# Optimization experiments

Measured on AMD Instinct MI355X. Metric: run time of the kernel, lower is better.

## Reference

```python
import jax, jax.numpy as jnp
import numpy as np

B, S, D, H = 4, 2048, 1024, 16
HD = D // H

def setup_inputs() -> dict:
    key = jax.random.key(0)
    ks = jax.random.split(key, 12)
    std = 1.0 / np.sqrt(D)
    inp = {
        'query': jax.random.normal(ks[0], (B, S, D), jnp.float32),
        'key':   jax.random.normal(ks[1], (B, S, D), jnp.float32),
        'value': jax.random.normal(ks[2], (B, S, D), jnp.float32),
        'mask':  jnp.tril(jnp.ones((S, S), jnp.int32))[None, None, :, :],  # [1,1,S,S] causal
        'Wq': jax.random.uniform(ks[3], (D, D), jnp.float32, -std, std),
        'bq': jax.random.uniform(ks[4], (D,), jnp.float32, -std, std),
        'Wk': jax.random.uniform(ks[5], (D, D), jnp.float32, -std, std),
        'bk': jax.random.uniform(ks[6], (D,), jnp.float32, -std, std),
        'Wv': jax.random.uniform(ks[7], (D, D), jnp.float32, -std, std),
        'bv': jax.random.uniform(ks[8], (D,), jnp.float32, -std, std),
        'Wo': jax.random.uniform(ks[9], (D, D), jnp.float32, -std, std),
        'bo': jax.random.uniform(ks[10], (D,), jnp.float32, -std, std),
    }
    return inp

def _split_heads(x, W, b):
    # torch Linear: x @ W.T + b ; then [B,S,H,HD] -> [B,H,S,HD]
    y = jnp.einsum('bsd,ed->bse', x, W) + b
    return y.reshape(x.shape[0], -1, H, HD).transpose(0, 2, 1, 3)

def reference(query, key, value, mask, Wq, bq, Wk, bk, Wv, bv, Wo, bo):
    q = _split_heads(query, Wq, bq)   # [B,H,S,HD]
    k = _split_heads(key,   Wk, bk)
    v = _split_heads(value, Wv, bv)
    logits = jnp.einsum('bhqd,bhkd->bhqk', q, k) / np.sqrt(HD)  # [B,H,S,S]
    logits = jnp.where(mask == 0, jnp.float32(-1e9), logits)
    attn = jax.nn.softmax(logits, axis=-1)
    out = jnp.einsum('bhqk,bhkd->bhqd', attn, v)               # [B,H,S,HD]
    out = out.transpose(0, 2, 1, 3).reshape(query.shape[0], -1, D)
    return jnp.einsum('bsd,ed->bse', out, Wo) + bo
```

## Files before the change

### kernel.cpp

```cpp
#include <hip/hip_runtime.h>
#include <hip/hip_bf16.h>


#define SLEN 2048
#define DMOD 1024

typedef __attribute__((ext_vector_type(8))) short s16x8;
typedef __attribute__((ext_vector_type(4))) float f32x4;

__device__ __forceinline__ unsigned short f2bf(float f) {
    union { __hip_bfloat16 h; unsigned short u; } cv;
    cv.h = __float2bfloat16(f);
    return cv.u;
}
__device__ __forceinline__ unsigned cvtpk(float a, float b) {
    unsigned r;
    asm("v_cvt_pk_bf16_f32 %0, %1, %2" : "=v"(r) : "v"(a), "v"(b));
    return r;
}

__device__ __forceinline__ void gload_lds16(const void* g, void* l) {
    __builtin_amdgcn_global_load_lds(
        (const __attribute__((address_space(1))) void*)g,
        (__attribute__((address_space(3))) void*)l, 16, 0, 0);
}

__global__ __launch_bounds__(256) void convert_w(
    const float* __restrict__ wq, const float* __restrict__ wk,
    const float* __restrict__ wv, const float* __restrict__ wo,
    unsigned short* __restrict__ dst)
{
    const int bid = blockIdx.x, tid = threadIdx.x;
    const int w = bid >> 7;
    const float* src = (w == 0) ? wq : (w == 1) ? wk : (w == 2) ? wv : wo;
    unsigned short* d = dst + (size_t)w * 1048576;
    const size_t off = (size_t)(bid & 127) * 8192;
#pragma unroll
    for (int i = 0; i < 8; ++i) {
        const size_t e = off + (size_t)(i * 256 + tid) * 4;
        float4 x = *reinterpret_cast<const float4*>(&src[e]);
        uint2 u;
        u.x = cvtpk(x.x, x.y);
        u.y = cvtpk(x.z, x.w);
        *reinterpret_cast<uint2*>(&d[e]) = u;
    }
}

template<int MODE>
__global__ __launch_bounds__(256) void gemm_qkv(
    const float* __restrict__ A, const unsigned short* __restrict__ W,
    const float* __restrict__ bias, unsigned short* __restrict__ outp,
    float oscale)
{
    __shared__ unsigned short Asm[2][8192];
    __shared__ unsigned short Bsm[2][8192];

    const int tid  = threadIdx.x;
    const int lane = tid & 63, wid = tid >> 6;
    const int l15 = lane & 15, lhi = lane >> 4;

    const int flat = blockIdx.x;
    const int logical = (flat & 7) * 64 + (flat >> 3);
    const int m0 = (logical >> 3) * 128, n0 = (logical & 7) * 128;
    const int wr = wid >> 1, wc = wid & 1;

    int soff[4];
    const float* aptc[4];
#pragma unroll
    for (int i = 0; i < 4; ++i) {
        const int f = i * 256 + tid;
        const int srow = f >> 3, sg = f & 7;
        soff[i] = srow * 128 + ((sg ^ (srow & 7)) * 16);
        aptc[i] = A + (size_t)(m0 + srow) * 1024 + sg * 8;
    }
    const int wsrow = lane >> 3;
    const int wsgr  = (lane & 7) ^ wsrow;
    const unsigned short* bpt = W + (size_t)(n0 + wid * 8 + wsrow) * 1024 + wsgr * 8;

    int aoff[2][4], boff[2][4];
#pragma unroll
    for (int kk = 0; kk < 2; ++kk)
#pragma unroll
        for (int i = 0; i < 4; ++i) {
            const int s = ((4 * kk + lhi) ^ (l15 & 7)) * 16;
            aoff[kk][i] = (wr * 64 + i * 16 + l15) * 128 + s;
            boff[kk][i] = (wc * 64 + i * 16 + l15) * 128 + s;
        }

    f32x4 acc[4][4];
#pragma unroll
    for (int i = 0; i < 4; ++i)
#pragma unroll
        for (int j = 0; j < 4; ++j) acc[i][j] = (f32x4)0.f;

    float4 aw[8];

    auto loadA = [&](int k0) {
#pragma unroll
        for (int i = 0; i < 4; ++i) {
            aw[2 * i]     = *reinterpret_cast<const float4*>(aptc[i] + k0);
            aw[2 * i + 1] = *reinterpret_cast<const float4*>(aptc[i] + k0 + 4);
        }
    };
    auto writeA = [&](int bsel) {
#pragma unroll
        for (int i = 0; i < 4; ++i) {
            uint4 u;
            u.x = cvtpk(aw[2 * i].x,     aw[2 * i].y);
            u.y = cvtpk(aw[2 * i].z,     aw[2 * i].w);
            u.z = cvtpk(aw[2 * i + 1].x, aw[2 * i + 1].y);
            u.w = cvtpk(aw[2 * i + 1].z, aw[2 * i + 1].w);
            *reinterpret_cast<uint4*>((char*)&Asm[bsel][0] + soff[i]) = u;
        }
    };
    auto stageW = [&](int bsel) {
        char* bd = (char*)Bsm + bsel * 16384 + wid * 1024;
#pragma unroll
        for (int i = 0; i < 4; ++i)
            gload_lds16(bpt + i * 32768, bd + i * 4096);
        bpt += 64;
    };

    loadA(0);
    stageW(0);
    writeA(0);
    __syncthreads();

#pragma unroll 1
    for (int kt = 0; kt < 16; ++kt) {
        if (kt < 15) {
            loadA((kt + 1) * 64);
            stageW((kt + 1) & 1);
        }
        const char* AB = (const char*)&Asm[kt & 1][0];
        const char* BB = (const char*)&Bsm[kt & 1][0];
#pragma unroll
        for (int kk = 0; kk < 2; ++kk) {
            s16x8 af[4], bfv[4];
#pragma unroll
            for (int i = 0; i < 4; ++i) af[i]  = *reinterpret_cast<const s16x8*>(AB + aoff[kk][i]);
#pragma unroll
            for (int j = 0; j < 4; ++j) bfv[j] = *reinterpret_cast<const s16x8*>(BB + boff[kk][j]);
#pragma unroll
            for (int i = 0; i < 4; ++i)
#pragma unroll
                for (int j = 0; j < 4; ++j)
                    acc[i][j] = __builtin_amdgcn_mfma_f32_16x16x32_bf16(af[i], bfv[j], acc[i][j], 0, 0, 0);
        }
        if (kt < 15) writeA((kt + 1) & 1);
        __syncthreads();
    }

#pragma unroll
    for (int j = 0; j < 4; ++j) {
        const int col = n0 + wc * 64 + j * 16 + l15;
        const float bv = bias[col];
#pragma unroll
        for (int i = 0; i < 4; ++i) {
#pragma unroll
            for (int r = 0; r < 4; ++r) {
                const int row = m0 + wr * 64 + i * 16 + lhi * 4 + r;
                const float val = (acc[i][j][r] + bv) * oscale;
                if constexpr (MODE == 0) {
                    outp[(size_t)((row >> 11) * 16 + (col >> 6)) * 131072
                         + (size_t)(row & 2047) * 64 + (col & 63)] = f2bf(val);
                } else {
                    outp[(size_t)((row >> 11) * 16 + (col >> 6)) * 131072
                         + (size_t)(col & 63) * 2048 + (row & 2047)] = f2bf(val);
                }
            }
        }
    }
}

__global__ __launch_bounds__(256) void gemm_out(
    const unsigned short* __restrict__ A, const unsigned short* __restrict__ W,
    const float* __restrict__ bias, float* __restrict__ outp)
{
    __shared__ unsigned short Asm[2][8192];
    __shared__ unsigned short Bsm[2][8192];

    const int tid  = threadIdx.x;
    const int lane = tid & 63, wid = tid >> 6;
    const int l15 = lane & 15, lhi = lane >> 4;

    const int flat = blockIdx.x;
    const int logical = (flat & 7) * 64 + (flat >> 3);
    const int m0 = (logical >> 3) * 128, n0 = (logical & 7) * 128;

    const int wr = wid >> 1, wc = wid & 1;
    const int srow = lane >> 3;
    const int sgr  = (lane & 7) ^ srow;

    int aoff[2][4], boff[2][4];
#pragma unroll
    for (int kk = 0; kk < 2; ++kk)
#pragma unroll
        for (int i = 0; i < 4; ++i) {
            const int s = ((4 * kk + lhi) ^ (l15 & 7)) * 16;
            aoff[kk][i] = (wr * 64 + i * 16 + l15) * 128 + s;
            boff[kk][i] = (wc * 64 + i * 16 + l15) * 128 + s;
        }

    const unsigned short* apt = A + (size_t)(m0 + wid * 8 + srow) * 1024 + sgr * 8;
    const unsigned short* bpt = W + (size_t)(n0 + wid * 8 + srow) * 1024 + sgr * 8;

    f32x4 acc[4][4];
#pragma unroll
    for (int i = 0; i < 4; ++i)
#pragma unroll
        for (int j = 0; j < 4; ++j) acc[i][j] = (f32x4)0.f;

    auto stage = [&](int bsel) {
        char* ad = (char*)Asm + bsel * 16384 + wid * 1024;
        char* bd = (char*)Bsm + bsel * 16384 + wid * 1024;
#pragma unroll
        for (int i = 0; i < 4; ++i) {
            gload_lds16(apt + i * 32768, ad + i * 4096);
            gload_lds16(bpt + i * 32768, bd + i * 4096);
        }
        apt += 64; bpt += 64;
    };

    stage(0);
    __syncthreads();
    int cur = 0;
#pragma unroll 1
    for (int kt = 0; kt < 16; ++kt) {
        if (kt < 15) stage(cur ^ 1);
        const char* AB = (const char*)Asm + cur * 16384;
        const char* BB = (const char*)Bsm + cur * 16384;
#pragma unroll
        for (int kk = 0; kk < 2; ++kk) {
            s16x8 af[4], bfv[4];
#pragma unroll
            for (int i = 0; i < 4; ++i) af[i]  = *reinterpret_cast<const s16x8*>(AB + aoff[kk][i]);
#pragma unroll
            for (int j = 0; j < 4; ++j) bfv[j] = *reinterpret_cast<const s16x8*>(BB + boff[kk][j]);
#pragma unroll
            for (int i = 0; i < 4; ++i)
#pragma unroll
                for (int j = 0; j < 4; ++j)
                    acc[i][j] = __builtin_amdgcn_mfma_f32_16x16x32_bf16(af[i], bfv[j], acc[i][j], 0, 0, 0);
        }
        __syncthreads();
        cur ^= 1;
    }

#pragma unroll
    for (int j = 0; j < 4; ++j) {
        const int col = n0 + wc * 64 + j * 16 + l15;
        const float bv = bias[col];
#pragma unroll
        for (int i = 0; i < 4; ++i)
#pragma unroll
            for (int r = 0; r < 4; ++r) {
                const int row = m0 + wr * 64 + i * 16 + lhi * 4 + r;
                outp[(size_t)row * 1024 + col] = acc[i][j][r] + bv;
            }
    }
}

#define EXPC 0.18033688011112043f

__global__ __launch_bounds__(256, 4) void attn_kernel(
    const unsigned short* __restrict__ Q,
    const unsigned short* __restrict__ Kc,
    const unsigned short* __restrict__ Vt,
    unsigned short* __restrict__ Ao)
{
    __shared__ char smem[40960];

    const int tid = threadIdx.x, lane = tid & 63, wid = tid >> 6;
    const int l15 = lane & 15, lhi = lane >> 4;
    const int sK = l15 & 7;
    const int sub = lane >> 3, c8s = lane & 7;
    const int thr = wid * 16 + l15;

    const int kb0 = l15 * 128 + (lhi ^ sK) * 16;
    const int kb1 = kb0 ^ 64;
    char* const pb0 = smem + 32768 + wid * 2048 + kb0;
    char* const pb1 = smem + 32768 + wid * 2048 + kb1;
    char* const PWp = smem + 32768 + wid * 2048;
    int pw[4];
#pragma unroll
    for (int nb = 0; nb < 4; ++nb)
        pw[nb] = (l15 * 16 + ((nb * 4 + lhi) ^ (2 * sK))) * 8;

    const int flat = blockIdx.x;
    const int logical = (flat & 7) * 128 + (flat >> 3);
    const int bx = logical & 15, bh = logical >> 4;
    const int qtL = bx, qtH = 31 - bx;
    const int q0L = qtL * 64, q0H = qtH * 64;

    const size_t base = (size_t)bh * SLEN * 64;
    const unsigned short* Qb = Q + base;
    const unsigned short* Kb = Kc + base;
    const unsigned short* Vb = Vt + base;
    const int b = bh >> 4, h = bh & 15;
    const int scol = (c8s ^ sub) * 8;

    const f32x4 fzero = (f32x4)0.f;
    const s16x8 onesb = (s16x8)(short)0x3F80;

    s16x8 aqL[2], aqH[2];
#pragma unroll
    for (int kk = 0; kk < 2; ++kk) {
        aqL[kk] = *reinterpret_cast<const s16x8*>(
            &Qb[(size_t)(q0L + wid * 16 + l15) * 64 + kk * 32 + 8 * lhi]);
        aqH[kk] = *reinterpret_cast<const s16x8*>(
            &Qb[(size_t)(q0H + wid * 16 + l15) * 64 + kk * 32 + 8 * lhi]);
    }

    f32x4 oL[4], oH[4];
#pragma unroll
    for (int nb = 0; nb < 4; ++nb) { oL[nb] = (f32x4)0.f; oH[nb] = (f32x4)0.f; }
    f32x4 lL = (f32x4)0.f, lH = (f32x4)0.f;

    const unsigned short* kpt = Kb + (16 * wid + sub) * 64 + scol;
    const unsigned short* vpt = Vb + (size_t)(16 * wid + sub) * SLEN + scol;

    auto stage = [&](int bsel) {
        char* kd = smem + bsel * 8192 + wid * 2048;
        char* vd = smem + 16384 + bsel * 8192 + wid * 2048;
        gload_lds16(kpt,         kd);
        gload_lds16(kpt + 512,   kd + 1024);
        gload_lds16(vpt,         vd);
        gload_lds16(vpt + 16384, vd + 1024);
        kpt += 4096; vpt += 64;
    };

    auto tile = [&](s16x8 (&aq)[2], f32x4 (&o_acc)[4], f32x4& l_acc,
                    bool domask, const char* c0, const char* c1) {
        f32x4 sc2[4];
        __builtin_amdgcn_s_setprio(1);
        {
            s16x8 ak[4];
#pragma unroll
            for (int nb = 0; nb < 4; ++nb)
                ak[nb] = *reinterpret_cast<const s16x8*>(c0 + nb * 2048);
#pragma unroll
            for (int nb = 0; nb < 4; ++nb)
                sc2[nb] = __builtin_amdgcn_mfma_f32_16x16x32_bf16(ak[nb], aq[0], fzero, 0, 0, 0);
#pragma unroll
            for (int nb = 0; nb < 4; ++nb)
                ak[nb] = *reinterpret_cast<const s16x8*>(c1 + nb * 2048);
#pragma unroll
            for (int nb = 0; nb < 4; ++nb)
                sc2[nb] = __builtin_amdgcn_mfma_f32_16x16x32_bf16(ak[nb], aq[1], sc2[nb], 0, 0, 0);
        }
        __builtin_amdgcn_s_setprio(0);

        if (domask) {
#pragma unroll
            for (int nb = 0; nb < 4; ++nb)
#pragma unroll
                for (int r = 0; r < 4; ++r)
                    if (nb * 16 + lhi * 4 + r > thr) sc2[nb][r] = -1e30f;
        }

#pragma unroll
        for (int nb = 0; nb < 4; ++nb) {
            float p0 = exp2f(sc2[nb][0]);
            float p1 = exp2f(sc2[nb][1]);
            float p2 = exp2f(sc2[nb][2]);
            float p3 = exp2f(sc2[nb][3]);
            uint2 u;
            u.x = cvtpk(p0, p1);
            u.y = cvtpk(p2, p3);
            *reinterpret_cast<uint2*>(PWp + pw[nb]) = u;
        }

        __builtin_amdgcn_s_setprio(1);
#pragma unroll
        for (int kk = 0; kk < 2; ++kk) {
            s16x8 pa = *reinterpret_cast<const s16x8*>(kk ? pb1 : pb0);
            const char* vb = (kk ? c1 : c0) + 16384;
            s16x8 bvv[4];
#pragma unroll
            for (int nb = 0; nb < 4; ++nb)
                bvv[nb] = *reinterpret_cast<const s16x8*>(vb + nb * 2048);
#pragma unroll
            for (int nb = 0; nb < 4; ++nb)
                o_acc[nb] = __builtin_amdgcn_mfma_f32_16x16x32_bf16(pa, bvv[nb], o_acc[nb], 0, 0, 0);
            l_acc = __builtin_amdgcn_mfma_f32_16x16x32_bf16(pa, onesb, l_acc, 0, 0, 0);
        }
        __builtin_amdgcn_s_setprio(0);
    };

    stage(0);
    __syncthreads();
    int cur = 0;
    const int nt = qtH + 1;

#pragma unroll 1
    for (int t = 0; t < nt; ++t) {
        if (t + 1 < nt) stage(cur ^ 1);
        const char* c0 = smem + cur * 8192 + kb0;
        const char* c1 = smem + cur * 8192 + kb1;
        if (t <= qtL) tile(aqL, oL, lL, t == qtL, c0, c1);
        tile(aqH, oH, lH, t == qtH, c0, c1);
        __syncthreads();
        cur ^= 1;
    }

    float liL[4], liH[4];
#pragma unroll
    for (int r = 0; r < 4; ++r) { liL[r] = 1.0f / lL[r]; liH[r] = 1.0f / lH[r]; }
#pragma unroll
    for (int nb = 0; nb < 4; ++nb)
#pragma unroll
        for (int r = 0; r < 4; ++r) {
            const int sL = q0L + wid * 16 + lhi * 4 + r;
            const int sH = q0H + wid * 16 + lhi * 4 + r;
            const size_t cix = h * 64 + nb * 16 + l15;
            Ao[((size_t)b * SLEN + sL) * DMOD + cix] = f2bf(oL[nb][r] * liL[r]);
            Ao[((size_t)b * SLEN + sH) * DMOD + cix] = f2bf(oH[nb][r] * liH[r]);
        }
}

extern "C" void kernel_launch(void* const* d_in, const int* in_sizes, int n_in,
                              void* d_out, int out_size, void* d_ws, size_t ws_size,
                              hipStream_t stream) {
    const float* q  = (const float*)d_in[0];
    const float* k  = (const float*)d_in[1];
    const float* v  = (const float*)d_in[2];
    const float* Wq = (const float*)d_in[4];
    const float* bq = (const float*)d_in[5];
    const float* Wk = (const float*)d_in[6];
    const float* bk = (const float*)d_in[7];
    const float* Wv = (const float*)d_in[8];
    const float* bv = (const float*)d_in[9];
    const float* Wo = (const float*)d_in[10];
    const float* bo = (const float*)d_in[11];

    unsigned short* wsp = (unsigned short*)d_ws;
    unsigned short* wqc = wsp;
    unsigned short* wkc = wsp + 1048576;
    unsigned short* wvc = wsp + 2097152;
    unsigned short* woc = wsp + 3145728;
    unsigned short* qb  = wsp + 4194304;
    unsigned short* kb  = wsp + 12582912;
    unsigned short* vtb = wsp + 20971520;
    unsigned short* ao  = wsp + 29360128;

    dim3 gb(256);
    convert_w<<<dim3(512), gb, 0, stream>>>(Wq, Wk, Wv, Wo, wsp);
    gemm_qkv<0><<<dim3(512), gb, 0, stream>>>(q, wqc, bq, qb, EXPC);
    gemm_qkv<0><<<dim3(512), gb, 0, stream>>>(k, wkc, bk, kb, 1.0f);
    gemm_qkv<1><<<dim3(512), gb, 0, stream>>>(v, wvc, bv, vtb, 1.0f);
    attn_kernel<<<dim3(1024), gb, 0, stream>>>(qb, kb, vtb, ao);
    gemm_out<<<dim3(512), gb, 0, stream>>>(ao, woc, bo, (float*)d_out);
}
```

Before: 174.8 us.

## Process four query tiles per attention block and double-register A loads in QKV GEMM

The attention kernel now gives each block four causally balanced query tiles (bx, 15-bx, 16+bx, 31-bx) instead of two. It stages 128 keys per iteration, so each K/V tile held in shared memory is reused across more queries, and the grid is halved to 512 blocks. The QKV GEMM splits its A prefetch into even and odd register sets and unrolls the k-loop by two, which fixes buffer indices and overlaps global loads for longer. The cost is more registers and shared memory (72KB), with occupancy hints dropped to 2 blocks per CU. That risks lower latency hiding and fewer blocks than CUs for balancing.

```diff
diff --git a/kernel.cpp b/kernel.cpp
--- a/kernel.cpp
+++ b/kernel.cpp
@@ -18,7 +18,6 @@
     asm("v_cvt_pk_bf16_f32 %0, %1, %2" : "=v"(r) : "v"(a), "v"(b));
     return r;
 }
-
 __device__ __forceinline__ void gload_lds16(const void* g, void* l) {
     __builtin_amdgcn_global_load_lds(
         (const __attribute__((address_space(1))) void*)g,
@@ -47,7 +46,7 @@
 }
 
 template<int MODE>
-__global__ __launch_bounds__(256) void gemm_qkv(
+__global__ __launch_bounds__(256, 2) void gemm_qkv(
     const float* __restrict__ A, const unsigned short* __restrict__ W,
     const float* __restrict__ bias, unsigned short* __restrict__ outp,
     float oscale)
@@ -93,16 +92,16 @@
 #pragma unroll
         for (int j = 0; j < 4; ++j) acc[i][j] = (f32x4)0.f;
 
-    float4 aw[8];
-
-    auto loadA = [&](int k0) {
+    float4 awE[8], awO[8];
+
+    auto loadTo = [&](float4 (&aw)[8], int k0) {
 #pragma unroll
         for (int i = 0; i < 4; ++i) {
             aw[2 * i]     = *reinterpret_cast<const float4*>(aptc[i] + k0);
             aw[2 * i + 1] = *reinterpret_cast<const float4*>(aptc[i] + k0 + 4);
         }
     };
-    auto writeA = [&](int bsel) {
+    auto writeFrom = [&](float4 (&aw)[8], int bsel) {
 #pragma unroll
         for (int i = 0; i < 4; ++i) {
             uint4 u;
@@ -120,20 +119,7 @@
             gload_lds16(bpt + i * 32768, bd + i * 4096);
         bpt += 64;
     };
-
-    loadA(0);
-    stageW(0);
-    writeA(0);
-    __syncthreads();
-
-#pragma unroll 1
-    for (int kt = 0; kt < 16; ++kt) {
-        if (kt < 15) {
-            loadA((kt + 1) * 64);
-            stageW((kt + 1) & 1);
-        }
-        const char* AB = (const char*)&Asm[kt & 1][0];
-        const char* BB = (const char*)&Bsm[kt & 1][0];
+    auto mfmaPhase = [&](const char* AB, const char* BB) {
 #pragma unroll
         for (int kk = 0; kk < 2; ++kk) {
             s16x8 af[4], bfv[4];
@@ -147,7 +133,25 @@
                 for (int j = 0; j < 4; ++j)
                     acc[i][j] = __builtin_amdgcn_mfma_f32_16x16x32_bf16(af[i], bfv[j], acc[i][j], 0, 0, 0);
         }
-        if (kt < 15) writeA((kt + 1) & 1);
+    };
+
+    loadTo(awE, 0);
+    stageW(0);
+    writeFrom(awE, 0);
+    loadTo(awO, 64);
+    __syncthreads();
+
+#pragma unroll 1
+    for (int kt = 0; kt < 16; kt += 2) {
+        if (kt + 2 < 16) loadTo(awE, (kt + 2) * 64);
+        if (kt + 1 < 16) stageW(1);
+        mfmaPhase((const char*)&Asm[0][0], (const char*)&Bsm[0][0]);
+        if (kt + 1 < 16) writeFrom(awO, 1);
+        __syncthreads();
+        if (kt + 3 < 16) loadTo(awO, (kt + 3) * 64);
+        if (kt + 2 < 16) stageW(0);
+        mfmaPhase((const char*)&Asm[1][0], (const char*)&Bsm[1][0]);
+        if (kt + 2 < 16) writeFrom(awE, 0);
         __syncthreads();
     }
 
@@ -263,13 +267,13 @@
 
 #define EXPC 0.18033688011112043f
 
-__global__ __launch_bounds__(256, 4) void attn_kernel(
+__global__ __launch_bounds__(256, 2) void attn_kernel(
     const unsigned short* __restrict__ Q,
     const unsigned short* __restrict__ Kc,
     const unsigned short* __restrict__ Vt,
     unsigned short* __restrict__ Ao)
 {
-    __shared__ char smem[40960];
+    __shared__ char smem[73728];
 
     const int tid = threadIdx.x, lane = tid & 63, wid = tid >> 6;
     const int l15 = lane & 15, lhi = lane >> 4;
@@ -279,19 +283,18 @@
 
     const int kb0 = l15 * 128 + (lhi ^ sK) * 16;
     const int kb1 = kb0 ^ 64;
-    char* const pb0 = smem + 32768 + wid * 2048 + kb0;
-    char* const pb1 = smem + 32768 + wid * 2048 + kb1;
-    char* const PWp = smem + 32768 + wid * 2048;
+    char* const pb0 = smem + 65536 + wid * 2048 + kb0;
+    char* const pb1 = smem + 65536 + wid * 2048 + kb1;
+    char* const PWp = smem + 65536 + wid * 2048;
     int pw[4];
 #pragma unroll
     for (int nb = 0; nb < 4; ++nb)
         pw[nb] = (l15 * 16 + ((nb * 4 + lhi) ^ (2 * sK))) * 8;
 
     const int flat = blockIdx.x;
-    const int logical = (flat & 7) * 128 + (flat >> 3);
-    const int bx = logical & 15, bh = logical >> 4;
-    const int qtL = bx, qtH = 31 - bx;
-    const int q0L = qtL * 64, q0H = qtH * 64;
+    const int logical = (flat & 7) * 64 + (flat >> 3);
+    const int bx = logical & 7, bh = logical >> 3;
+    const int qts[4] = {bx, 15 - bx, 16 + bx, 31 - bx};
 
     const size_t base = (size_t)bh * SLEN * 64;
     const unsigned short* Qb = Q + base;
@@ -303,34 +306,37 @@
     const f32x4 fzero = (f32x4)0.f;
     const s16x8 onesb = (s16x8)(short)0x3F80;
 
-    s16x8 aqL[2], aqH[2];
-#pragma unroll
-    for (int kk = 0; kk < 2; ++kk) {
-        aqL[kk] = *reinterpret_cast<const s16x8*>(
-            &Qb[(size_t)(q0L + wid * 16 + l15) * 64 + kk * 32 + 8 * lhi]);
-        aqH[kk] = *reinterpret_cast<const s16x8*>(
-            &Qb[(size_t)(q0H + wid * 16 + l15) * 64 + kk * 32 + 8 * lhi]);
-    }
-
-    f32x4 oL[4], oH[4];
-#pragma unroll
-    for (int nb = 0; nb < 4; ++nb) { oL[nb] = (f32x4)0.f; oH[nb] = (f32x4)0.f; }
-    f32x4 lL = (f32x4)0.f, lH = (f32x4)0.f;
+    s16x8 aq[4][2];
+    f32x4 oA[4][4], lA[4];
+#pragma unroll
+    for (int j = 0; j < 4; ++j) {
+#pragma unroll
+        for (int kk = 0; kk < 2; ++kk)
+            aq[j][kk] = *reinterpret_cast<const s16x8*>(
+                &Qb[(size_t)(qts[j] * 64 + wid * 16 + l15) * 64 + kk * 32 + 8 * lhi]);
+#pragma unroll
+        for (int nb = 0; nb < 4; ++nb) oA[j][nb] = (f32x4)0.f;
+        lA[j] = (f32x4)0.f;
+    }
 
     const unsigned short* kpt = Kb + (16 * wid + sub) * 64 + scol;
     const unsigned short* vpt = Vb + (size_t)(16 * wid + sub) * SLEN + scol;
 
     auto stage = [&](int bsel) {
-        char* kd = smem + bsel * 8192 + wid * 2048;
-        char* vd = smem + 16384 + bsel * 8192 + wid * 2048;
-        gload_lds16(kpt,         kd);
-        gload_lds16(kpt + 512,   kd + 1024);
-        gload_lds16(vpt,         vd);
-        gload_lds16(vpt + 16384, vd + 1024);
-        kpt += 4096; vpt += 64;
-    };
-
-    auto tile = [&](s16x8 (&aq)[2], f32x4 (&o_acc)[4], f32x4& l_acc,
+        char* kd = smem + bsel * 16384 + wid * 2048;
+        char* vd = smem + 32768 + bsel * 16384 + wid * 2048;
+        gload_lds16(kpt,                kd);
+        gload_lds16(kpt + 512,          kd + 1024);
+        gload_lds16(kpt + 4096,         kd + 8192);
+        gload_lds16(kpt + 4096 + 512,   kd + 8192 + 1024);
+        gload_lds16(vpt,                vd);
+        gload_lds16(vpt + 16384,        vd + 1024);
+        gload_lds16(vpt + 64,           vd + 8192);
+        gload_lds16(vpt + 16384 + 64,   vd + 8192 + 1024);
+        kpt += 8192; vpt += 128;
+    };
+
+    auto tile = [&](const s16x8 (&aqj)[2], f32x4 (&o_acc)[4], f32x4& l_acc,
                     bool domask, const char* c0, const char* c1) {
         f32x4 sc2[4];
         __builtin_amdgcn_s_setprio(1);
@@ -341,13 +347,13 @@
                 ak[nb] = *reinterpret_cast<const s16x8*>(c0 + nb * 2048);
 #pragma unroll
             for (int nb = 0; nb < 4; ++nb)
-                sc2[nb] = __builtin_amdgcn_mfma_f32_16x16x32_bf16(ak[nb], aq[0], fzero, 0, 0, 0);
+                sc2[nb] = __builtin_amdgcn_mfma_f32_16x16x32_bf16(ak[nb], aqj[0], fzero, 0, 0, 0);
 #pragma unroll
             for (int nb = 0; nb < 4; ++nb)
                 ak[nb] = *reinterpret_cast<const s16x8*>(c1 + nb * 2048);
 #pragma unroll
             for (int nb = 0; nb < 4; ++nb)
-                sc2[nb] = __builtin_amdgcn_mfma_f32_16x16x32_bf16(ak[nb], aq[1], sc2[nb], 0, 0, 0);
+                sc2[nb] = __builtin_amdgcn_mfma_f32_16x16x32_bf16(ak[nb], aqj[1], sc2[nb], 0, 0, 0);
         }
         __builtin_amdgcn_s_setprio(0);
 
@@ -375,7 +381,7 @@
 #pragma unroll
         for (int kk = 0; kk < 2; ++kk) {
             s16x8 pa = *reinterpret_cast<const s16x8*>(kk ? pb1 : pb0);
-            const char* vb = (kk ? c1 : c0) + 16384;
+            const char* vb = (kk ? c1 : c0) + 32768;
             s16x8 bvv[4];
 #pragma unroll
             for (int nb = 0; nb < 4; ++nb)
@@ -391,32 +397,40 @@
     stage(0);
     __syncthreads();
     int cur = 0;
-    const int nt = qtH + 1;
+    const int nt = (33 - bx) >> 1;
 
 #pragma unroll 1
     for (int t = 0; t < nt; ++t) {
         if (t + 1 < nt) stage(cur ^ 1);
-        const char* c0 = smem + cur * 8192 + kb0;
-        const char* c1 = smem + cur * 8192 + kb1;
-        if (t <= qtL) tile(aqL, oL, lL, t == qtL, c0, c1);
-        tile(aqH, oH, lH, t == qtH, c0, c1);
+        const char* kbase = smem + cur * 16384;
+#pragma unroll
+        for (int st = 0; st < 2; ++st) {
+            const int k64 = 2 * t + st;
+            const char* c0 = kbase + st * 8192 + kb0;
+            const char* c1 = kbase + st * 8192 + kb1;
+#pragma unroll
+            for (int j = 0; j < 4; ++j)
+                if (k64 <= qts[j])
+                    tile(aq[j], oA[j], lA[j], k64 == qts[j], c0, c1);
+        }
         __syncthreads();
         cur ^= 1;
     }
 
-    float liL[4], liH[4];
-#pragma unroll
-    for (int r = 0; r < 4; ++r) { liL[r] = 1.0f / lL[r]; liH[r] = 1.0f / lH[r]; }
-#pragma unroll
-    for (int nb = 0; nb < 4; ++nb)
-#pragma unroll
-        for (int r = 0; r < 4; ++r) {
-            const int sL = q0L + wid * 16 + lhi * 4 + r;
-            const int sH = q0H + wid * 16 + lhi * 4 + r;
-            const size_t cix = h * 64 + nb * 16 + l15;
-            Ao[((size_t)b * SLEN + sL) * DMOD + cix] = f2bf(oL[nb][r] * liL[r]);
-            Ao[((size_t)b * SLEN + sH) * DMOD + cix] = f2bf(oH[nb][r] * liH[r]);
-        }
+#pragma unroll
+    for (int j = 0; j < 4; ++j) {
+        float li[4];
+#pragma unroll
+        for (int r = 0; r < 4; ++r) li[r] = 1.0f / lA[j][r];
+#pragma unroll
+        for (int nb = 0; nb < 4; ++nb)
+#pragma unroll
+            for (int r = 0; r < 4; ++r) {
+                const int s = qts[j] * 64 + wid * 16 + lhi * 4 + r;
+                Ao[((size_t)b * SLEN + s) * DMOD + h * 64 + nb * 16 + l15] =
+                    f2bf(oA[j][nb][r] * li[r]);
+            }
+    }
 }
 
 extern "C" void kernel_launch(void* const* d_in, const int* in_sizes, int n_in,
@@ -449,6 +463,6 @@
     gemm_qkv<0><<<dim3(512), gb, 0, stream>>>(q, wqc, bq, qb, EXPC);
     gemm_qkv<0><<<dim3(512), gb, 0, stream>>>(k, wkc, bk, kb, 1.0f);
     gemm_qkv<1><<<dim3(512), gb, 0, stream>>>(v, wvc, bv, vtb, 1.0f);
-    attn_kernel<<<dim3(1024), gb, 0, stream>>>(qb, kb, vtb, ao);
+    attn_kernel<<<dim3(512), gb, 0, stream>>>(qb, kb, vtb, ao);
     gemm_out<<<dim3(512), gb, 0, stream>>>(ao, woc, bo, (float*)d_out);
 }
```

Result: slower. 182.2 us (+4.2%).

## Deepen QKV GEMM A-operand prefetch to two stages with manual waitcnt barriers

Applied to the files above, without the earlier changes.

The QKV projection GEMM loop is unrolled by two and uses two register buffers for the fp32 A tiles, so global loads are issued two k-steps ahead. It replaces __syncthreads with explicit s_waitcnt vmcnt(8) plus s_barrier, so the most recent loads can stay in flight across the barrier. It also adds a minimum-blocks hint of 2 to launch_bounds. This aims to hide global load latency better, at the cost of more registers and correctness that now depends on the hand-counted vmcnt value matching the number of outstanding loads.

```diff
diff --git a/kernel.cpp b/kernel.cpp
--- a/kernel.cpp
+++ b/kernel.cpp
@@ -18,7 +18,6 @@
     asm("v_cvt_pk_bf16_f32 %0, %1, %2" : "=v"(r) : "v"(a), "v"(b));
     return r;
 }
-
 __device__ __forceinline__ void gload_lds16(const void* g, void* l) {
     __builtin_amdgcn_global_load_lds(
         (const __attribute__((address_space(1))) void*)g,
@@ -47,7 +46,7 @@
 }
 
 template<int MODE>
-__global__ __launch_bounds__(256) void gemm_qkv(
+__global__ __launch_bounds__(256, 2) void gemm_qkv(
     const float* __restrict__ A, const unsigned short* __restrict__ W,
     const float* __restrict__ bias, unsigned short* __restrict__ outp,
     float oscale)
@@ -93,16 +92,16 @@
 #pragma unroll
         for (int j = 0; j < 4; ++j) acc[i][j] = (f32x4)0.f;
 
-    float4 aw[8];
-
-    auto loadA = [&](int k0) {
+    float4 awE[8], awO[8];
+
+    auto loadTo = [&](float4 (&aw)[8], int k0) {
 #pragma unroll
         for (int i = 0; i < 4; ++i) {
             aw[2 * i]     = *reinterpret_cast<const float4*>(aptc[i] + k0);
             aw[2 * i + 1] = *reinterpret_cast<const float4*>(aptc[i] + k0 + 4);
         }
     };
-    auto writeA = [&](int bsel) {
+    auto writeFrom = [&](float4 (&aw)[8], int bsel) {
 #pragma unroll
         for (int i = 0; i < 4; ++i) {
             uint4 u;
@@ -120,20 +119,7 @@
             gload_lds16(bpt + i * 32768, bd + i * 4096);
         bpt += 64;
     };
-
-    loadA(0);
-    stageW(0);
-    writeA(0);
-    __syncthreads();
-
-#pragma unroll 1
-    for (int kt = 0; kt < 16; ++kt) {
-        if (kt < 15) {
-            loadA((kt + 1) * 64);
-            stageW((kt + 1) & 1);
-        }
-        const char* AB = (const char*)&Asm[kt & 1][0];
-        const char* BB = (const char*)&Bsm[kt & 1][0];
+    auto mfmaPhase = [&](const char* AB, const char* BB) {
 #pragma unroll
         for (int kk = 0; kk < 2; ++kk) {
             s16x8 af[4], bfv[4];
@@ -147,8 +133,36 @@
                 for (int j = 0; j < 4; ++j)
                     acc[i][j] = __builtin_amdgcn_mfma_f32_16x16x32_bf16(af[i], bfv[j], acc[i][j], 0, 0, 0);
         }
-        if (kt < 15) writeA((kt + 1) & 1);
-        __syncthreads();
+    };
+    auto barrier8 = [&]() {
+        asm volatile("s_waitcnt vmcnt(8) lgkmcnt(0)" ::: "memory");
+        __builtin_amdgcn_s_barrier();
+        __builtin_amdgcn_sched_barrier(0);
+    };
+    auto barrier0 = [&]() {
+        asm volatile("s_waitcnt vmcnt(0) lgkmcnt(0)" ::: "memory");
+        __builtin_amdgcn_s_barrier();
+        __builtin_amdgcn_sched_barrier(0);
+    };
+
+    loadTo(awE, 0);
+    stageW(0);
+    writeFrom(awE, 0);
+    loadTo(awO, 64);
+    barrier8();
+
+#pragma unroll 1
+    for (int kt = 0; kt < 16; kt += 2) {
+        if (kt + 1 < 16) stageW(1);
+        if (kt + 2 < 16) loadTo(awE, (kt + 2) * 64);
+        mfmaPhase((const char*)&Asm[0][0], (const char*)&Bsm[0][0]);
+        if (kt + 1 < 16) writeFrom(awO, 1);
+        if (kt + 2 < 16) barrier8(); else barrier0();
+        if (kt + 2 < 16) stageW(0);
+        if (kt + 3 < 16) loadTo(awO, (kt + 3) * 64);
+        mfmaPhase((const char*)&Asm[1][0], (const char*)&Bsm[1][0]);
+        if (kt + 2 < 16) writeFrom(awE, 0);
+        if (kt + 3 < 16) barrier8(); else barrier0();
     }
 
 #pragma unroll
```

New measurement: 170.3 us (median of 3 runs). 1.03x faster.
